# Optimization experiments

Hardware: AMD Instinct MI355X
Metric: run time of the kernel (lower is better)

The kernel has to match this reference:

```python
import jax, jax.numpy as jnp
import numpy as np

GROUPS = 4
KLD_SCALE = 10.0
COMMITMENT_COST = 0.25


def setup_inputs() -> dict:
    key = jax.random.key(0)
    k1, k2 = jax.random.split(key)
    z = jax.random.normal(k1, (8, 4096, 512), dtype=jnp.float32)
    embed_w = jax.random.normal(k2, (512, 128), dtype=jnp.float32)
    return {"z": z, "embed_w": embed_w}


def reference(z, embed_w):
    B, N, D = z.shape
    d = D // GROUPS  # sub-vector dim per group
    flat = z.reshape(B * N * GROUPS, d)  # [M, d]
    # squared euclidean distance to each codebook entry: [M, K]
    dist = (
        jnp.sum(flat * flat, axis=1, keepdims=True)
        - 2.0 * flat @ embed_w.T
        + jnp.sum(embed_w * embed_w, axis=1)[None, :]
    )
    ind = jnp.argmin(dist, axis=1)  # argmax(-dist)
    z_q = embed_w[ind]  # [M, d] codebook gather
    sg = jax.lax.stop_gradient
    diff = KLD_SCALE * (
        COMMITMENT_COST * jnp.mean((sg(z_q) - flat) ** 2)
        + jnp.mean((z_q - sg(flat)) ** 2)
    )
    # straight-through estimator
    z_q_st = (flat + sg(z_q - flat)).reshape(B, N, D)
    ind_out = ind.reshape(N, B, GROUPS)  # matches torch .view on contiguous buffer
    return (z_q_st, diff, ind_out)
```

## Files before the change

### kernel.cpp

```cpp
#include <hip/hip_runtime.h>
#include <float.h>


typedef _Float16 half8 __attribute__((ext_vector_type(8)));
typedef __attribute__((ext_vector_type(4))) float f32x4;

constexpr int Dn = 128;
constexpr int K  = 512;
constexpr long long Mrows = 131072;
constexpr int RPW   = 32;
constexpr int WAVES = 16;
constexpr int RPB   = RPW * WAVES;
constexpr int NBLK  = (int)(Mrows / RPB);
constexpr float TAU_A = 0.05f;

constexpr size_t ZQ_SIZE  = (size_t)Mrows * Dn;
constexpr size_t DIFF_OFF = ZQ_SIZE;
constexpr size_t IND_OFF  = ZQ_SIZE + 1;

__device__ inline void gload_lds16(const void* g, void* l) {
    __builtin_amdgcn_global_load_lds(
        (const __attribute__((address_space(1))) unsigned int*)g,
        (__attribute__((address_space(3))) unsigned int*)l,
        16, 0, 0);
}

__global__ void wnorm_kernel(const float* __restrict__ W, float* __restrict__ wn2) {
    int k = blockIdx.x * blockDim.x + threadIdx.x;
    if (k < K) {
        double s = 0.0;
        const float* w = W + (size_t)k * Dn;
        #pragma unroll 4
        for (int i = 0; i < Dn; ++i) { double v = (double)w[i]; s += v * v; }
        wn2[k] = (float)(-0.5 * s);
    }
}

__global__ void prep_kernel(const float* __restrict__ W, unsigned short* __restrict__ Wp) {
    int t = blockIdx.x * 256 + threadIdx.x;
    int code = t >> 4;
    int gs   = t & 15;
    int g    = gs ^ (code & 7);
    const float* src = W + (size_t)code * Dn + g * 8;
    ushort4 h[2];
    #pragma unroll
    for (int half = 0; half < 2; ++half) {
        float4 v = *(const float4*)(src + half * 4);
        float vv[4] = {v.x, v.y, v.z, v.w};
        unsigned short* hp = (unsigned short*)&h[half];
        #pragma unroll
        for (int e = 0; e < 4; ++e) {
            _Float16 hh = (_Float16)vv[e];
            hp[e] = __builtin_bit_cast(unsigned short, hh);
        }
    }
    size_t base = (size_t)t * 8;
    *(ushort4*)(Wp + base)     = h[0];
    *(ushort4*)(Wp + base + 4) = h[1];
}

__global__ __launch_bounds__(1024, 4) void vq_main(
        const float* __restrict__ Z, const float* __restrict__ W,
        const unsigned short* __restrict__ Wp, const float* __restrict__ wn2,
        float* __restrict__ out, double* __restrict__ diffsum) {
    __shared__ __align__(16) char Wlds[131072];
    __shared__ float wn2_s[K];
    __shared__ float xn_s[RPB];
    __shared__ int   sIdx[RPB];
    __shared__ int   flagList[RPB];
    __shared__ int   flagN;
    __shared__ float wpart[WAVES];

    const int tid  = threadIdx.x;
    const int w    = tid >> 6;
    const int lane = tid & 63;
    const int lm   = lane & 15;
    const int lg   = lane >> 4;
    const size_t row0 = (size_t)blockIdx.x * RPB;

    if (tid == 0) flagN = 0;

    {
        const char* gsrc = (const char*)Wp;
        #pragma unroll
        for (int it = 0; it < 8; ++it) {
            const int gbase = it * 1024 + w * 64;
            gload_lds16(gsrc + (size_t)(gbase + lane) * 16, Wlds + (size_t)gbase * 16);
        }
    }
    if (tid < K) wn2_s[tid] = wn2[tid];

    half8 ah[2][4];
    #pragma unroll
    for (int r = 0; r < 2; ++r) {
        const size_t grow = row0 + (size_t)w * RPW + r * 16 + lm;
        float s2 = 0.f;
        #pragma unroll
        for (int ks = 0; ks < 4; ++ks) {
            const float* xp = Z + grow * Dn + ks * 32 + lg * 8;
            float4 x0 = *(const float4*)xp;
            float4 x1 = *(const float4*)(xp + 4);
            float xv[8] = {x0.x, x0.y, x0.z, x0.w, x1.x, x1.y, x1.z, x1.w};
            #pragma unroll
            for (int j = 0; j < 8; ++j) {
                ah[r][ks][j] = (_Float16)xv[j];
                s2 += xv[j] * xv[j];
            }
        }
        s2 += __shfl_xor(s2, 16);
        s2 += __shfl_xor(s2, 32);
        if (lg == 0) xn_s[w * RPW + r * 16 + lm] = s2;
    }

    float m1[2][4], m2[2][4];
    int   i1[2][4];
    #pragma unroll
    for (int r = 0; r < 2; ++r)
        #pragma unroll
        for (int j = 0; j < 4; ++j) { m1[r][j] = -FLT_MAX; m2[r][j] = -FLT_MAX; i1[r][j] = 0; }

    asm volatile("s_waitcnt vmcnt(0)" ::: "memory");
    __syncthreads();

    #pragma unroll 2
    for (int t = 0; t < 32; ++t) {
        const int code = t * 16 + lm;
        const float cinit = wn2_s[code];
        half8 bh[4];
        #pragma unroll
        for (int ks = 0; ks < 4; ++ks) {
            const int off = code * 256 + ((((ks << 2) + lg) ^ (code & 7)) << 4);
            bh[ks] = *(const half8*)(Wlds + off);
        }
        f32x4 acc[2];
        #pragma unroll
        for (int r = 0; r < 2; ++r) acc[r] = (f32x4){cinit, cinit, cinit, cinit};
        #pragma unroll
        for (int ks = 0; ks < 4; ++ks) {
            #pragma unroll
            for (int r = 0; r < 2; ++r)
                acc[r] = __builtin_amdgcn_mfma_f32_16x16x32_f16(ah[r][ks], bh[ks], acc[r], 0, 0, 0);
        }
        #pragma unroll
        for (int r = 0; r < 2; ++r) {
            #pragma unroll
            for (int j = 0; j < 4; ++j) {
                const float a = acc[r][j];
                m2[r][j] = __builtin_amdgcn_fmed3f(a, m1[r][j], m2[r][j]);
                const bool gt = a > m1[r][j];
                m1[r][j] = fmaxf(m1[r][j], a);
                i1[r][j] = gt ? code : i1[r][j];
            }
        }
    }

    #pragma unroll
    for (int sft = 1; sft < 16; sft <<= 1) {
        #pragma unroll
        for (int r = 0; r < 2; ++r) {
            #pragma unroll
            for (int j = 0; j < 4; ++j) {
                float o1 = __shfl_xor(m1[r][j], sft);
                float o2 = __shfl_xor(m2[r][j], sft);
                int   oi = __shfl_xor(i1[r][j], sft);
                if (o1 > m1[r][j] || (o1 == m1[r][j] && oi < i1[r][j])) {
                    m2[r][j] = fmaxf(m1[r][j], o2);
                    m1[r][j] = o1;
                    i1[r][j] = oi;
                } else {
                    m2[r][j] = fmaxf(m2[r][j], o1);
                }
            }
        }
    }

    float psum = 0.f;
    if (lm == 0) {
        #pragma unroll
        for (int r = 0; r < 2; ++r) {
            #pragma unroll
            for (int j = 0; j < 4; ++j) {
                const int row = w * RPW + r * 16 + lg * 4 + j;
                sIdx[row] = i1[r][j];
                psum += xn_s[row] - 2.f * m1[r][j];
                if (m1[r][j] - m2[r][j] < TAU_A) {
                    int pos = atomicAdd(&flagN, 1);
                    flagList[pos] = row;
                }
            }
        }
    }
    __syncthreads();

    {
        const int nflag = flagN;
        const int cg    = lane >> 3;
        const int dbase = (lane & 7) * 16;
        for (int fi = w; fi < nflag; fi += WAVES) {
            const int rr = flagList[fi];
            const float* xp = Z + (row0 + rr) * Dn + dbase;
            double xd[16];
            #pragma unroll
            for (int q = 0; q < 16; q += 4) {
                float4 v = *(const float4*)(xp + q);
                xd[q] = v.x; xd[q+1] = v.y; xd[q+2] = v.z; xd[q+3] = v.w;
            }
            double best = 1e300; int bi = 0;
            for (int cb = 0; cb < 64; ++cb) {
                const int c = cb * 8 + cg;
                const float* wp = W + (size_t)c * Dn + dbase;
                double s = 0.0;
                #pragma unroll
                for (int q = 0; q < 16; q += 4) {
                    float4 wv = *(const float4*)(wp + q);
                    double d0 = xd[q]   - (double)wv.x;
                    double d1 = xd[q+1] - (double)wv.y;
                    double d2 = xd[q+2] - (double)wv.z;
                    double d3 = xd[q+3] - (double)wv.w;
                    s += d0 * d0 + d1 * d1 + d2 * d2 + d3 * d3;
                }
                s += __shfl_xor(s, 1);
                s += __shfl_xor(s, 2);
                s += __shfl_xor(s, 4);
                if (s < best) { best = s; bi = c; }
            }
            #pragma unroll
            for (int sft = 8; sft < 64; sft <<= 1) {
                double ob = __shfl_xor(best, sft);
                int    ok = __shfl_xor(bi, sft);
                if (ob < best || (ob == best && ok < bi)) { best = ob; bi = ok; }
            }
            if (lane == 0) sIdx[rr] = bi;
        }
    }
    __syncthreads();

    #pragma unroll
    for (int it = 0; it < 16; ++it) {
        int f4i = tid + it * 1024;
        int row = f4i >> 5, cq = f4i & 31;
        int ind = sIdx[row];
        float4 wv = ((const float4*)(W + (size_t)ind * Dn))[cq];
        ((float4*)(out + (row0 + row) * Dn))[cq] = wv;
    }
    if (tid < RPB) out[IND_OFF + row0 + tid] = (float)sIdx[tid];

    #pragma unroll
    for (int sft = 1; sft < 64; sft <<= 1) psum += __shfl_xor(psum, sft);
    if (lane == 0) wpart[w] = psum;
    __syncthreads();
    if (tid == 0) {
        double t = 0.0;
        #pragma unroll
        for (int i = 0; i < WAVES; ++i) t += (double)wpart[i];
        atomicAdd(diffsum, t);
    }
}

__global__ void diff_kernel(const double* __restrict__ diffsum, float* __restrict__ out) {
    if (threadIdx.x == 0 && blockIdx.x == 0) {
        out[DIFF_OFF] = (float)(12.5 * diffsum[0] / (double)ZQ_SIZE);
    }
}

extern "C" void kernel_launch(void* const* d_in, const int* in_sizes, int n_in,
                              void* d_out, int out_size, void* d_ws, size_t ws_size,
                              hipStream_t stream) {
    (void)in_sizes; (void)n_in; (void)out_size; (void)ws_size;
    const float* Z = (const float*)d_in[0];
    const float* W = (const float*)d_in[1];
    float* out = (float*)d_out;
    double* diffsum = (double*)d_ws;
    float* wn2 = (float*)((char*)d_ws + 16);
    unsigned short* Wp = (unsigned short*)((char*)d_ws + 4096);

    hipMemsetAsync(d_ws, 0, 16, stream);
    wnorm_kernel<<<2, 256, 0, stream>>>(W, wn2);
    prep_kernel<<<32, 256, 0, stream>>>(W, Wp);
    vq_main<<<NBLK, 1024, 0, stream>>>(Z, W, Wp, wn2, out, diffsum);
    diff_kernel<<<1, 64, 0, stream>>>(diffsum, out);
}
```

Measured before the change: 112.9 us.

## Fuse codebook prep into main kernel and make fallback and epilogue per-wave

Removes the separate norm and fp16-packing kernels: each block now converts the fp32 codebook to swizzled fp16 in LDS itself and computes the code norms in fp32 instead of double. Flagged-row refinement becomes per-wave via a ballot over a flag array, so the block-level atomics, the flag list and two block barriers go away. The gather epilogue and the diff reduction are done per wave, with one double atomic per wave instead of per block. The code-tile loop start is staggered per wave to spread LDS bank traffic. The trade is redundant codebook conversion in every block, more global atomics, and uneven fallback work across waves with no block-level balancing.

```diff
diff --git a/kernel.cpp b/kernel.cpp
--- a/kernel.cpp
+++ b/kernel.cpp
@@ -18,58 +18,14 @@
 constexpr size_t DIFF_OFF = ZQ_SIZE;
 constexpr size_t IND_OFF  = ZQ_SIZE + 1;
 
-__device__ inline void gload_lds16(const void* g, void* l) {
-    __builtin_amdgcn_global_load_lds(
-        (const __attribute__((address_space(1))) unsigned int*)g,
-        (__attribute__((address_space(3))) unsigned int*)l,
-        16, 0, 0);
-}
-
-__global__ void wnorm_kernel(const float* __restrict__ W, float* __restrict__ wn2) {
-    int k = blockIdx.x * blockDim.x + threadIdx.x;
-    if (k < K) {
-        double s = 0.0;
-        const float* w = W + (size_t)k * Dn;
-        #pragma unroll 4
-        for (int i = 0; i < Dn; ++i) { double v = (double)w[i]; s += v * v; }
-        wn2[k] = (float)(-0.5 * s);
-    }
-}
-
-__global__ void prep_kernel(const float* __restrict__ W, unsigned short* __restrict__ Wp) {
-    int t = blockIdx.x * 256 + threadIdx.x;
-    int code = t >> 4;
-    int gs   = t & 15;
-    int g    = gs ^ (code & 7);
-    const float* src = W + (size_t)code * Dn + g * 8;
-    ushort4 h[2];
-    #pragma unroll
-    for (int half = 0; half < 2; ++half) {
-        float4 v = *(const float4*)(src + half * 4);
-        float vv[4] = {v.x, v.y, v.z, v.w};
-        unsigned short* hp = (unsigned short*)&h[half];
-        #pragma unroll
-        for (int e = 0; e < 4; ++e) {
-            _Float16 hh = (_Float16)vv[e];
-            hp[e] = __builtin_bit_cast(unsigned short, hh);
-        }
-    }
-    size_t base = (size_t)t * 8;
-    *(ushort4*)(Wp + base)     = h[0];
-    *(ushort4*)(Wp + base + 4) = h[1];
-}
-
 __global__ __launch_bounds__(1024, 4) void vq_main(
         const float* __restrict__ Z, const float* __restrict__ W,
-        const unsigned short* __restrict__ Wp, const float* __restrict__ wn2,
         float* __restrict__ out, double* __restrict__ diffsum) {
     __shared__ __align__(16) char Wlds[131072];
     __shared__ float wn2_s[K];
     __shared__ float xn_s[RPB];
     __shared__ int   sIdx[RPB];
-    __shared__ int   flagList[RPB];
-    __shared__ int   flagN;
-    __shared__ float wpart[WAVES];
+    __shared__ int   sFlag[RPB];
 
     const int tid  = threadIdx.x;
     const int w    = tid >> 6;
@@ -78,17 +34,27 @@
     const int lg   = lane >> 4;
     const size_t row0 = (size_t)blockIdx.x * RPB;
 
-    if (tid == 0) flagN = 0;
-
     {
-        const char* gsrc = (const char*)Wp;
-        #pragma unroll
-        for (int it = 0; it < 8; ++it) {
-            const int gbase = it * 1024 + w * 64;
-            gload_lds16(gsrc + (size_t)(gbase + lane) * 16, Wlds + (size_t)gbase * 16);
-        }
-    }
-    if (tid < K) wn2_s[tid] = wn2[tid];
+        const int code = tid >> 1, h = tid & 1;
+        const float4* ws4 = (const float4*)(W + (size_t)code * Dn + h * 64);
+        float s2 = 0.f;
+        #pragma unroll
+        for (int g8 = 0; g8 < 8; ++g8) {
+            float4 a = ws4[g8 * 2];
+            float4 b = ws4[g8 * 2 + 1];
+            float vv[8] = {a.x, a.y, a.z, a.w, b.x, b.y, b.z, b.w};
+            half8 hv;
+            #pragma unroll
+            for (int j = 0; j < 8; ++j) {
+                hv[j] = (_Float16)vv[j];
+                s2 += vv[j] * vv[j];
+            }
+            const int g = h * 8 + g8;
+            *(half8*)(Wlds + code * 256 + ((g ^ (code & 7)) << 4)) = hv;
+        }
+        s2 += __shfl_xor(s2, 1);
+        if (!h) wn2_s[code] = -0.5f * s2;
+    }
 
     half8 ah[2][4];
     #pragma unroll
@@ -119,11 +85,12 @@
         #pragma unroll
         for (int j = 0; j < 4; ++j) { m1[r][j] = -FLT_MAX; m2[r][j] = -FLT_MAX; i1[r][j] = 0; }
 
-    asm volatile("s_waitcnt vmcnt(0)" ::: "memory");
     __syncthreads();
 
+    const int t0 = (w * 2) & 31;
     #pragma unroll 2
-    for (int t = 0; t < 32; ++t) {
+    for (int ti = 0; ti < 32; ++ti) {
+        const int t = (ti + t0) & 31;
         const int code = t * 16 + lm;
         const float cinit = wn2_s[code];
         half8 bh[4];
@@ -181,24 +148,21 @@
             #pragma unroll
             for (int j = 0; j < 4; ++j) {
                 const int row = w * RPW + r * 16 + lg * 4 + j;
-                sIdx[row] = i1[r][j];
+                sIdx[row]  = i1[r][j];
+                sFlag[row] = (m1[r][j] - m2[r][j] < TAU_A) ? 1 : 0;
                 psum += xn_s[row] - 2.f * m1[r][j];
-                if (m1[r][j] - m2[r][j] < TAU_A) {
-                    int pos = atomicAdd(&flagN, 1);
-                    flagList[pos] = row;
-                }
-            }
-        }
-    }
-    __syncthreads();
+            }
+        }
+    }
 
     {
-        const int nflag = flagN;
         const int cg    = lane >> 3;
         const int dbase = (lane & 7) * 16;
-        for (int fi = w; fi < nflag; fi += WAVES) {
-            const int rr = flagList[fi];
-            const float* xp = Z + (row0 + rr) * Dn + dbase;
+        unsigned long long fl = __ballot(lane < 32 && sFlag[w * RPW + (lane & 31)] != 0);
+        while (fl) {
+            const int rr = __ffsll(fl) - 1;
+            fl &= fl - 1;
+            const float* xp = Z + (row0 + w * RPW + rr) * Dn + dbase;
             double xd[16];
             #pragma unroll
             for (int q = 0; q < 16; q += 4) {
@@ -230,31 +194,24 @@
                 int    ok = __shfl_xor(bi, sft);
                 if (ob < best || (ob == best && ok < bi)) { best = ob; bi = ok; }
             }
-            if (lane == 0) sIdx[rr] = bi;
-        }
-    }
-    __syncthreads();
+            if (lane == 0) sIdx[w * RPW + rr] = bi;
+        }
+    }
 
     #pragma unroll
     for (int it = 0; it < 16; ++it) {
-        int f4i = tid + it * 1024;
-        int row = f4i >> 5, cq = f4i & 31;
-        int ind = sIdx[row];
+        int f4i = lane + it * 64;
+        int rl  = f4i >> 5, cq = f4i & 31;
+        int ind = sIdx[w * RPW + rl];
         float4 wv = ((const float4*)(W + (size_t)ind * Dn))[cq];
-        ((float4*)(out + (row0 + row) * Dn))[cq] = wv;
-    }
-    if (tid < RPB) out[IND_OFF + row0 + tid] = (float)sIdx[tid];
+        ((float4*)(out + (row0 + w * RPW + rl) * Dn))[cq] = wv;
+    }
+    if (lane < RPW)
+        out[IND_OFF + row0 + w * RPW + lane] = (float)sIdx[w * RPW + lane];
 
     #pragma unroll
     for (int sft = 1; sft < 64; sft <<= 1) psum += __shfl_xor(psum, sft);
-    if (lane == 0) wpart[w] = psum;
-    __syncthreads();
-    if (tid == 0) {
-        double t = 0.0;
-        #pragma unroll
-        for (int i = 0; i < WAVES; ++i) t += (double)wpart[i];
-        atomicAdd(diffsum, t);
-    }
+    if (lane == 0) atomicAdd(diffsum, (double)psum);
 }
 
 __global__ void diff_kernel(const double* __restrict__ diffsum, float* __restrict__ out) {
@@ -271,12 +228,8 @@
     const float* W = (const float*)d_in[1];
     float* out = (float*)d_out;
     double* diffsum = (double*)d_ws;
-    float* wn2 = (float*)((char*)d_ws + 16);
-    unsigned short* Wp = (unsigned short*)((char*)d_ws + 4096);
 
     hipMemsetAsync(d_ws, 0, 16, stream);
-    wnorm_kernel<<<2, 256, 0, stream>>>(W, wn2);
-    prep_kernel<<<32, 256, 0, stream>>>(W, Wp);
-    vq_main<<<NBLK, 1024, 0, stream>>>(Z, W, Wp, wn2, out, diffsum);
+    vq_main<<<NBLK, 1024, 0, stream>>>(Z, W, out, diffsum);
     diff_kernel<<<1, 64, 0, stream>>>(diffsum, out);
 }
```

After: 158.9 us. 1.41x slower.
